# Kernel optimization log

Measured on AMD Instinct MI355X. Metric: run time of the kernel, lower is better.

Reference implementation:

```python
import jax, jax.numpy as jnp
import numpy as np

K = 3          # kernel size (hardcoded in module)
PAD = 1        # kernel_size // 2
K2 = K * K


def conv3x3(x, w, b):
    """Standard 3x3 stride-1 same-padding conv, NCHW / OIHW."""
    y = jax.lax.conv_general_dilated(
        x, w, window_strides=(1, 1), padding=[(PAD, PAD), (PAD, PAD)],
        dimension_numbers=('NCHW', 'OIHW', 'NCHW'))
    return y + b[None, :, None, None]


def setup_inputs() -> dict:
    key = jax.random.key(0)
    ks = jax.random.split(key, 8)
    B, C, O, H, W = 8, 64, 64, 128, 128
    x = jax.random.normal(ks[0], (B, C, H, W), dtype=jnp.float32)
    # offset conv: 2*K2 output channels; small init so offsets stay modest
    w_off = jax.random.normal(ks[1], (2 * K2, C, K, K), dtype=jnp.float32) * 0.05
    b_off = jnp.zeros((2 * K2,), dtype=jnp.float32)
    # modulator conv: K2 output channels
    w_mod = jax.random.normal(ks[2], (K2, C, K, K), dtype=jnp.float32) * 0.05
    b_mod = jnp.zeros((K2,), dtype=jnp.float32)
    # main deformable conv weight/bias
    w = jax.random.normal(ks[3], (O, C, K, K), dtype=jnp.float32) * (1.0 / np.sqrt(C * K2))
    b = jax.random.normal(ks[4], (O,), dtype=jnp.float32) * 0.01
    return {"x": x, "w_off": w_off, "b_off": b_off,
            "w_mod": w_mod, "b_mod": b_mod, "w": w, "b": b}


def reference(x, w_off, b_off, w_mod, b_mod, w, b):
    B, C, H, W = x.shape
    O = w.shape[0]

    # offset / modulator heads (torchvision layout: channel 2k = dy, 2k+1 = dx)
    offset = conv3x3(x, w_off, b_off)                       # [B, 2*K2, H, W]
    mask = 2.0 * jax.nn.sigmoid(conv3x3(x, w_mod, b_mod))   # [B, K2, H, W]
    off = offset.reshape(B, K2, 2, H, W)
    dy, dx = off[:, :, 0], off[:, :, 1]                     # [B, K2, H, W]

    # base sampling grid: p = (h - pad + ki, w - pad + kj) + learned offset
    ki = (jnp.arange(K2) // K).astype(x.dtype)
    kj = (jnp.arange(K2) % K).astype(x.dtype)
    hh = jnp.arange(H, dtype=x.dtype)
    ww = jnp.arange(W, dtype=x.dtype)
    py = dy + hh[None, None, :, None] - PAD + ki[None, :, None, None]
    px = dx + ww[None, None, None, :] - PAD + kj[None, :, None, None]

    def sample_one(x_b, py_b, px_b):
        # x_b: [C, H, W]; py_b, px_b: [K2, H, W]. Bilinear, zero outside.
        y0 = jnp.floor(py_b)
        x0 = jnp.floor(px_b)
        wy = py_b - y0                                      # [K2, H, W]
        wx = px_b - x0
        y0i = y0.astype(jnp.int32)
        x0i = x0.astype(jnp.int32)

        def gather(yi, xi):
            valid = (yi >= 0) & (yi < H) & (xi >= 0) & (xi < W)
            v = x_b[:, jnp.clip(yi, 0, H - 1), jnp.clip(xi, 0, W - 1)]  # [C,K2,H,W]
            return v * valid[None].astype(x_b.dtype)

        v00 = gather(y0i, x0i)
        v01 = gather(y0i, x0i + 1)
        v10 = gather(y0i + 1, x0i)
        v11 = gather(y0i + 1, x0i + 1)
        return (v00 * (1 - wy) * (1 - wx) + v01 * (1 - wy) * wx
                + v10 * wy * (1 - wx) + v11 * wy * wx)       # [C, K2, H, W]

    sampled = jax.vmap(sample_one)(x, py, px)               # [B, C, K2, H, W]

    # modulated contraction over (c, k): GEMM-like core
    wk = w.reshape(O, C, K2)
    out = jnp.einsum('bckhw,bkhw,ock->bohw', sampled, mask, wk)
    return out + b[None, :, None, None]
```

## Files before the change

### kernel.cpp

```cpp
#include <hip/hip_runtime.h>
#include <math.h>

#define H_ 128
#define W_ 128
#define C_ 64
#define O_ 64
#define B_ 8
#define K2_ 9
#define HWSZ (H_*W_)

typedef float f2u __attribute__((ext_vector_type(2), aligned(4)));

__global__ __launch_bounds__(256) void prep_weights_k(
    const float* __restrict__ w, const float* __restrict__ w_off,
    const float* __restrict__ w_mod, float* __restrict__ wt,
    float* __restrict__ wom) {
    int id = blockIdx.x * 256 + threadIdx.x;
    if (id < K2_ * C_ * O_) {
        int o = id & (O_ - 1);
        int c = (id >> 6) & (C_ - 1);
        int k = id / (C_ * O_);
        wt[id] = w[(o * C_ + c) * K2_ + k];
    }
    int id2 = id - K2_ * C_ * O_;
    if (id2 >= 0 && id2 < C_ * 243) {
        int k = id2 % 9;
        int tt = (id2 / 9) % 27;
        int c = id2 / 243;
        float v = (tt < 18) ? w_off[(tt * C_ + c) * K2_ + k]
                            : w_mod[((tt - 18) * C_ + c) * K2_ + k];
        wom[id2] = v;
    }
}

__global__ __launch_bounds__(512) void conv_offmask_k(
    const float* __restrict__ x,
    const float* __restrict__ wom, const float* __restrict__ b_off,
    const float* __restrict__ b_mod,
    float* __restrict__ pyA, float* __restrict__ pxA, float* __restrict__ mA) {
    __shared__ float red[27 * 128];

    int b     = blockIdx.x & 7;
    int strip = blockIdx.x >> 3;
    int tid   = threadIdx.x;
    int t     = tid & 127;
    int q     = tid >> 7;
    int c0    = __builtin_amdgcn_readfirstlane(q << 4);
    int p     = strip * 128 + t;
    int w     = p & (W_ - 1);
    int h     = p >> 7;

    int offs[9];
    float valid[9];
#pragma unroll
    for (int i = 0; i < 9; i++) {
        int dy = i / 3 - 1, dx = i % 3 - 1;
        int yy = h + dy, xx = w + dx;
        bool v = (yy >= 0 && yy < H_ && xx >= 0 && xx < W_);
        int yc = min(max(yy, 0), H_ - 1);
        int xc = min(max(xx, 0), W_ - 1);
        offs[i] = yc * W_ + xc;
        valid[i] = v ? 1.0f : 0.0f;
    }

    float acc[27];
#pragma unroll
    for (int o = 0; o < 27; o++) acc[o] = 0.0f;

    const float* xb = x + (b * C_ + c0) * HWSZ;

    float v[9];
#pragma unroll
    for (int i = 0; i < 9; i++) v[i] = xb[offs[i]] * valid[i];

    for (int c = 0; c < 16; c++) {
        const float* xn = xb + min(c + 1, 15) * HWSZ;
        float vn[9];
#pragma unroll
        for (int i = 0; i < 9; i++) vn[i] = xn[offs[i]] * valid[i];

        const float* wc = wom + (c0 + c) * 243;
#pragma unroll
        for (int o = 0; o < 27; o++) {
#pragma unroll
            for (int kk = 0; kk < 9; kk++) acc[o] += v[kk] * wc[o * 9 + kk];
        }
#pragma unroll
        for (int i = 0; i < 9; i++) v[i] = vn[i];
    }

    if (q == 3) {
#pragma unroll
        for (int o = 0; o < 27; o++) red[o * 128 + t] = acc[o];
    }
    __syncthreads();
    if (q == 2) {
#pragma unroll
        for (int o = 0; o < 27; o++) red[o * 128 + t] += acc[o];
    }
    __syncthreads();
    if (q == 1) {
#pragma unroll
        for (int o = 0; o < 27; o++) red[o * 128 + t] += acc[o];
    }
    __syncthreads();
    if (q == 0) {
#pragma unroll
        for (int k = 0; k < 9; k++) {
            float dy = acc[2 * k]     + red[(2 * k)     * 128 + t] + b_off[2 * k];
            float dx = acc[2 * k + 1] + red[(2 * k + 1) * 128 + t] + b_off[2 * k + 1];
            float mm = acc[18 + k]    + red[(18 + k)    * 128 + t] + b_mod[k];
            float mask = 2.0f / (1.0f + __expf(-mm));
            float py = dy + (float)h - 1.0f + (float)(k / 3);
            float px = dx + (float)w - 1.0f + (float)(k % 3);
            int idx = (b * 9 + k) * HWSZ + p;
            pyA[idx] = py;
            pxA[idx] = px;
            mA[idx] = mask;
        }
    }
}

__global__ __launch_bounds__(512) void sample_gemm_k(
    const float* __restrict__ x,
    const float* __restrict__ pyA, const float* __restrict__ pxA,
    const float* __restrict__ mA, const float* __restrict__ wt,
    const float* __restrict__ bias, float* __restrict__ out) {
    __shared__ float red[O_ * 256];

    int b     = blockIdx.x & 7;
    int strip = blockIdx.x >> 3;
    int tid   = threadIdx.x;
    int t     = tid & 255;
    int half  = tid >> 8;
    int c0    = __builtin_amdgcn_readfirstlane(half << 5);
    int p     = strip * 256 + t;

    float acc[O_];
#pragma unroll
    for (int o = 0; o < O_; o++) acc[o] = 0.0f;

    const float* xb = x + (b * C_ + c0) * HWSZ;

    for (int k = 0; k < 9; k++) {
        int idx = (b * 9 + k) * HWSZ + p;
        float py = pyA[idx];
        float px = pxA[idx];
        float m  = mA[idx];

        float y0f = floorf(py), x0f = floorf(px);
        float wy = py - y0f, wx = px - x0f;
        int y0 = (int)y0f, x0 = (int)x0f;
        int y1 = y0 + 1;
        float vy0 = (y0 >= 0 && y0 < H_) ? 1.0f : 0.0f;
        float vy1 = (y1 >= 0 && y1 < H_) ? 1.0f : 0.0f;
        float vx0 = (x0 >= 0 && x0 < W_) ? 1.0f : 0.0f;
        float vx1 = (x0 >= -1 && x0 < W_ - 1) ? 1.0f : 0.0f;
        int y0c = min(max(y0, 0), H_ - 1), y1c = min(max(y1, 0), H_ - 1);

        float w00 = (1.0f - wy) * (1.0f - wx) * vy0 * vx0 * m;
        float w01 = (1.0f - wy) * wx * vy0 * vx1 * m;
        float w10 = wy * (1.0f - wx) * vy1 * vx0 * m;
        float w11 = wy * wx * vy1 * vx1 * m;

        int lc   = min(max(x0, 0), W_ - 2);
        bool xlo = (x0 < 0);
        bool xhi = (x0 > W_ - 2);
        float a00 = xhi ? 0.0f : (xlo ? w01 : w00);
        float a01 = xlo ? 0.0f : (xhi ? w00 : w01);
        float a10 = xhi ? 0.0f : (xlo ? w11 : w10);
        float a11 = xlo ? 0.0f : (xhi ? w10 : w11);

        int r0 = y0c * W_ + lc;
        int r1 = y1c * W_ + lc;

        const float* wp = wt + k * (C_ * O_) + c0 * O_;
        for (int c = 0; c < 32; c++) {
            const float* xc = xb + c * HWSZ;
            f2u f0 = *(const f2u*)(xc + r0);
            f2u f1 = *(const f2u*)(xc + r1);
            float s = a00 * f0.x + a01 * f0.y + a10 * f1.x + a11 * f1.y;
            const float* wpc = wp + c * O_;
#pragma unroll
            for (int o = 0; o < O_; o++) acc[o] += s * wpc[o];
        }
    }

    if (half) {
#pragma unroll
        for (int o = 0; o < O_; o++) red[o * 256 + t] = acc[o];
    }
    __syncthreads();
    if (!half) {
        int obase = b * O_ * HWSZ + p;
#pragma unroll
        for (int o = 0; o < O_; o++)
            out[obase + o * HWSZ] = acc[o] + red[o * 256 + t] + bias[o];
    }
}

extern "C" void kernel_launch(void* const* d_in, const int* in_sizes, int n_in,
                              void* d_out, int out_size, void* d_ws, size_t ws_size,
                              hipStream_t stream) {
    const float* x     = (const float*)d_in[0];
    const float* w_off = (const float*)d_in[1];
    const float* b_off = (const float*)d_in[2];
    const float* w_mod = (const float*)d_in[3];
    const float* b_mod = (const float*)d_in[4];
    const float* w     = (const float*)d_in[5];
    const float* bias  = (const float*)d_in[6];
    float* out = (float*)d_out;

    const int nCoord = B_ * K2_ * HWSZ;
    float* pyA = (float*)d_ws;
    float* pxA = pyA + nCoord;
    float* mA  = pxA + nCoord;
    float* wt  = mA + nCoord;
    float* wom = wt + K2_ * C_ * O_;

    const int nPrep = K2_ * C_ * O_ + C_ * 243;
    hipLaunchKernelGGL(prep_weights_k, dim3((nPrep + 255) / 256), dim3(256),
                       0, stream, w, w_off, w_mod, wt, wom);
    hipLaunchKernelGGL(conv_offmask_k, dim3(1024), dim3(512), 0, stream,
                       x, wom, b_off, b_mod, pyA, pxA, mA);
    hipLaunchKernelGGL(sample_gemm_k, dim3(512), dim3(512), 0, stream,
                       x, pyA, pxA, mA, wt, bias, out);
}
```

Baseline: 321.6 us.

## Fuse offset/mask conv into deformable sampling GEMM kernel via shared memory

Merges the offset/modulator convolution kernel into the sampling+GEMM kernel. Each block first computes py/px/mask for its 256 pixels over two channel halves, reduces them in LDS, and keeps them there instead of writing them to global workspace. This removes a launch and the global round-trip of three B*9*H*W arrays. In exchange, the conv stage now runs on only 512 blocks with 32 channels per thread rather than 1024 blocks with 16, so it has less parallelism. The added launch-bounds occupancy hint may also pressure registers given the 64-wide accumulator.

```diff
diff --git a/kernel.cpp b/kernel.cpp
--- a/kernel.cpp
+++ b/kernel.cpp
@@ -33,98 +33,10 @@
     }
 }
 
-__global__ __launch_bounds__(512) void conv_offmask_k(
+__global__ __launch_bounds__(512, 4) void deform_fused_k(
     const float* __restrict__ x,
     const float* __restrict__ wom, const float* __restrict__ b_off,
-    const float* __restrict__ b_mod,
-    float* __restrict__ pyA, float* __restrict__ pxA, float* __restrict__ mA) {
-    __shared__ float red[27 * 128];
-
-    int b     = blockIdx.x & 7;
-    int strip = blockIdx.x >> 3;
-    int tid   = threadIdx.x;
-    int t     = tid & 127;
-    int q     = tid >> 7;
-    int c0    = __builtin_amdgcn_readfirstlane(q << 4);
-    int p     = strip * 128 + t;
-    int w     = p & (W_ - 1);
-    int h     = p >> 7;
-
-    int offs[9];
-    float valid[9];
-#pragma unroll
-    for (int i = 0; i < 9; i++) {
-        int dy = i / 3 - 1, dx = i % 3 - 1;
-        int yy = h + dy, xx = w + dx;
-        bool v = (yy >= 0 && yy < H_ && xx >= 0 && xx < W_);
-        int yc = min(max(yy, 0), H_ - 1);
-        int xc = min(max(xx, 0), W_ - 1);
-        offs[i] = yc * W_ + xc;
-        valid[i] = v ? 1.0f : 0.0f;
-    }
-
-    float acc[27];
-#pragma unroll
-    for (int o = 0; o < 27; o++) acc[o] = 0.0f;
-
-    const float* xb = x + (b * C_ + c0) * HWSZ;
-
-    float v[9];
-#pragma unroll
-    for (int i = 0; i < 9; i++) v[i] = xb[offs[i]] * valid[i];
-
-    for (int c = 0; c < 16; c++) {
-        const float* xn = xb + min(c + 1, 15) * HWSZ;
-        float vn[9];
-#pragma unroll
-        for (int i = 0; i < 9; i++) vn[i] = xn[offs[i]] * valid[i];
-
-        const float* wc = wom + (c0 + c) * 243;
-#pragma unroll
-        for (int o = 0; o < 27; o++) {
-#pragma unroll
-            for (int kk = 0; kk < 9; kk++) acc[o] += v[kk] * wc[o * 9 + kk];
-        }
-#pragma unroll
-        for (int i = 0; i < 9; i++) v[i] = vn[i];
-    }
-
-    if (q == 3) {
-#pragma unroll
-        for (int o = 0; o < 27; o++) red[o * 128 + t] = acc[o];
-    }
-    __syncthreads();
-    if (q == 2) {
-#pragma unroll
-        for (int o = 0; o < 27; o++) red[o * 128 + t] += acc[o];
-    }
-    __syncthreads();
-    if (q == 1) {
-#pragma unroll
-        for (int o = 0; o < 27; o++) red[o * 128 + t] += acc[o];
-    }
-    __syncthreads();
-    if (q == 0) {
-#pragma unroll
-        for (int k = 0; k < 9; k++) {
-            float dy = acc[2 * k]     + red[(2 * k)     * 128 + t] + b_off[2 * k];
-            float dx = acc[2 * k + 1] + red[(2 * k + 1) * 128 + t] + b_off[2 * k + 1];
-            float mm = acc[18 + k]    + red[(18 + k)    * 128 + t] + b_mod[k];
-            float mask = 2.0f / (1.0f + __expf(-mm));
-            float py = dy + (float)h - 1.0f + (float)(k / 3);
-            float px = dx + (float)w - 1.0f + (float)(k % 3);
-            int idx = (b * 9 + k) * HWSZ + p;
-            pyA[idx] = py;
-            pxA[idx] = px;
-            mA[idx] = mask;
-        }
-    }
-}
-
-__global__ __launch_bounds__(512) void sample_gemm_k(
-    const float* __restrict__ x,
-    const float* __restrict__ pyA, const float* __restrict__ pxA,
-    const float* __restrict__ mA, const float* __restrict__ wt,
+    const float* __restrict__ b_mod, const float* __restrict__ wt,
     const float* __restrict__ bias, float* __restrict__ out) {
     __shared__ float red[O_ * 256];
 
@@ -135,18 +47,79 @@
     int half  = tid >> 8;
     int c0    = __builtin_amdgcn_readfirstlane(half << 5);
     int p     = strip * 256 + t;
+    int w     = p & (W_ - 1);
+    int h     = p >> 7;
+
+    const float* xb = x + (b * C_ + c0) * HWSZ;
+
+    {
+        int offs[9];
+        float valid[9];
+#pragma unroll
+        for (int i = 0; i < 9; i++) {
+            int dy = i / 3 - 1, dx = i % 3 - 1;
+            int yy = h + dy, xx = w + dx;
+            bool v = (yy >= 0 && yy < H_ && xx >= 0 && xx < W_);
+            int yc = min(max(yy, 0), H_ - 1);
+            int xc = min(max(xx, 0), W_ - 1);
+            offs[i] = yc * W_ + xc;
+            valid[i] = v ? 1.0f : 0.0f;
+        }
+
+        float acc27[27];
+#pragma unroll
+        for (int o = 0; o < 27; o++) acc27[o] = 0.0f;
+
+        float v[9];
+#pragma unroll
+        for (int i = 0; i < 9; i++) v[i] = xb[offs[i]] * valid[i];
+
+        for (int c = 0; c < 32; c++) {
+            const float* xn = xb + min(c + 1, 31) * HWSZ;
+            float vn[9];
+#pragma unroll
+            for (int i = 0; i < 9; i++) vn[i] = xn[offs[i]] * valid[i];
+
+            const float* wc = wom + (c0 + c) * 243;
+#pragma unroll
+            for (int o = 0; o < 27; o++) {
+#pragma unroll
+                for (int kk = 0; kk < 9; kk++) acc27[o] += v[kk] * wc[o * 9 + kk];
+            }
+#pragma unroll
+            for (int i = 0; i < 9; i++) v[i] = vn[i];
+        }
+
+        if (half) {
+#pragma unroll
+            for (int o = 0; o < 27; o++) red[o * 256 + t] = acc27[o];
+        }
+        __syncthreads();
+        if (!half) {
+#pragma unroll
+            for (int k = 0; k < 9; k++) {
+                float dy = acc27[2 * k]     + red[(2 * k)     * 256 + t] + b_off[2 * k];
+                float dx = acc27[2 * k + 1] + red[(2 * k + 1) * 256 + t] + b_off[2 * k + 1];
+                float mm = acc27[18 + k]    + red[(18 + k)    * 256 + t] + b_mod[k];
+                float mask = 2.0f / (1.0f + __expf(-mm));
+                float py = dy + (float)h - 1.0f + (float)(k / 3);
+                float px = dx + (float)w - 1.0f + (float)(k % 3);
+                red[(27 + 3 * k + 0) * 256 + t] = py;
+                red[(27 + 3 * k + 1) * 256 + t] = px;
+                red[(27 + 3 * k + 2) * 256 + t] = mask;
+            }
+        }
+        __syncthreads();
+    }
 
     float acc[O_];
 #pragma unroll
     for (int o = 0; o < O_; o++) acc[o] = 0.0f;
 
-    const float* xb = x + (b * C_ + c0) * HWSZ;
-
     for (int k = 0; k < 9; k++) {
-        int idx = (b * 9 + k) * HWSZ + p;
-        float py = pyA[idx];
-        float px = pxA[idx];
-        float m  = mA[idx];
+        float py = red[(27 + 3 * k + 0) * 256 + t];
+        float px = red[(27 + 3 * k + 1) * 256 + t];
+        float m  = red[(27 + 3 * k + 2) * 256 + t];
 
         float y0f = floorf(py), x0f = floorf(px);
         float wy = py - y0f, wx = px - x0f;
@@ -186,6 +159,7 @@
         }
     }
 
+    __syncthreads();
     if (half) {
 #pragma unroll
         for (int o = 0; o < O_; o++) red[o * 256 + t] = acc[o];
@@ -211,18 +185,12 @@
     const float* bias  = (const float*)d_in[6];
     float* out = (float*)d_out;
 
-    const int nCoord = B_ * K2_ * HWSZ;
-    float* pyA = (float*)d_ws;
-    float* pxA = pyA + nCoord;
-    float* mA  = pxA + nCoord;
-    float* wt  = mA + nCoord;
+    float* wt  = (float*)d_ws;
     float* wom = wt + K2_ * C_ * O_;
 
     const int nPrep = K2_ * C_ * O_ + C_ * 243;
     hipLaunchKernelGGL(prep_weights_k, dim3((nPrep + 255) / 256), dim3(256),
                        0, stream, w, w_off, w_mod, wt, wom);
-    hipLaunchKernelGGL(conv_offmask_k, dim3(1024), dim3(512), 0, stream,
-                       x, wom, b_off, b_mod, pyA, pxA, mA);
-    hipLaunchKernelGGL(sample_gemm_k, dim3(512), dim3(512), 0, stream,
-                       x, pyA, pxA, mA, wt, bias, out);
+    hipLaunchKernelGGL(deform_fused_k, dim3(512), dim3(512), 0, stream,
+                       x, wom, b_off, b_mod, wt, bias, out);
 }
```

After: 350.7 us. 9.1% more time.

## Split offset conv by output channels and compute two rows per block

Applied to the files above, without the earlier changes.

The offset/mask conv kernel now divides work across the four thread groups by output channel (7 of 28 padded outputs each) rather than by input channel. Each thread computes two output rows, reusing a 4x3 input window across both. This removes the serial three-stage shared-memory reduction and halves the block count. The weight layout is padded to 28 outputs, and each thread now loops over all 64 input channels with fewer accumulators, so there are more loads per thread but better reuse of input rows.

```diff
diff --git a/kernel.cpp b/kernel.cpp
--- a/kernel.cpp
+++ b/kernel.cpp
@@ -23,99 +23,100 @@
         wt[id] = w[(o * C_ + c) * K2_ + k];
     }
     int id2 = id - K2_ * C_ * O_;
-    if (id2 >= 0 && id2 < C_ * 243) {
+    if (id2 >= 0 && id2 < C_ * 252) {
         int k = id2 % 9;
-        int tt = (id2 / 9) % 27;
-        int c = id2 / 243;
-        float v = (tt < 18) ? w_off[(tt * C_ + c) * K2_ + k]
-                            : w_mod[((tt - 18) * C_ + c) * K2_ + k];
+        int tt = (id2 / 9) % 28;
+        int c = id2 / 252;
+        float v = 0.0f;
+        if (tt < 18)      v = w_off[(tt * C_ + c) * K2_ + k];
+        else if (tt < 27) v = w_mod[((tt - 18) * C_ + c) * K2_ + k];
         wom[id2] = v;
     }
 }
 
-__global__ __launch_bounds__(512) void conv_offmask_k(
+__global__ __launch_bounds__(512, 4) void conv_offmask_k(
     const float* __restrict__ x,
     const float* __restrict__ wom, const float* __restrict__ b_off,
     const float* __restrict__ b_mod,
     float* __restrict__ pyA, float* __restrict__ pxA, float* __restrict__ mA) {
-    __shared__ float red[27 * 128];
+    __shared__ float AO[28 * 256];
 
     int b     = blockIdx.x & 7;
     int strip = blockIdx.x >> 3;
     int tid   = threadIdx.x;
     int t     = tid & 127;
     int q     = tid >> 7;
-    int c0    = __builtin_amdgcn_readfirstlane(q << 4);
-    int p     = strip * 128 + t;
-    int w     = p & (W_ - 1);
-    int h     = p >> 7;
-
-    int offs[9];
-    float valid[9];
-#pragma unroll
-    for (int i = 0; i < 9; i++) {
-        int dy = i / 3 - 1, dx = i % 3 - 1;
-        int yy = h + dy, xx = w + dx;
-        bool v = (yy >= 0 && yy < H_ && xx >= 0 && xx < W_);
-        int yc = min(max(yy, 0), H_ - 1);
-        int xc = min(max(xx, 0), W_ - 1);
-        offs[i] = yc * W_ + xc;
-        valid[i] = v ? 1.0f : 0.0f;
-    }
-
-    float acc[27];
-#pragma unroll
-    for (int o = 0; o < 27; o++) acc[o] = 0.0f;
-
-    const float* xb = x + (b * C_ + c0) * HWSZ;
-
-    float v[9];
-#pragma unroll
-    for (int i = 0; i < 9; i++) v[i] = xb[offs[i]] * valid[i];
-
-    for (int c = 0; c < 16; c++) {
-        const float* xn = xb + min(c + 1, 15) * HWSZ;
-        float vn[9];
-#pragma unroll
-        for (int i = 0; i < 9; i++) vn[i] = xn[offs[i]] * valid[i];
-
-        const float* wc = wom + (c0 + c) * 243;
-#pragma unroll
-        for (int o = 0; o < 27; o++) {
-#pragma unroll
-            for (int kk = 0; kk < 9; kk++) acc[o] += v[kk] * wc[o * 9 + kk];
-        }
-#pragma unroll
-        for (int i = 0; i < 9; i++) v[i] = vn[i];
-    }
-
-    if (q == 3) {
-#pragma unroll
-        for (int o = 0; o < 27; o++) red[o * 128 + t] = acc[o];
+    int qu    = __builtin_amdgcn_readfirstlane(q);
+    int h0    = strip * 2;
+
+    int offs[12]; float valid[12];
+#pragma unroll
+    for (int r = 0; r < 4; r++) {
+#pragma unroll
+        for (int cx = 0; cx < 3; cx++) {
+            int yy = h0 - 1 + r, xx = t - 1 + cx;
+            bool vv = (yy >= 0 && yy < H_ && xx >= 0 && xx < W_);
+            int yc = min(max(yy, 0), H_ - 1);
+            int xc = min(max(xx, 0), W_ - 1);
+            offs[r * 3 + cx] = yc * W_ + xc;
+            valid[r * 3 + cx] = vv ? 1.0f : 0.0f;
+        }
+    }
+
+    float acc0[7], acc1[7];
+#pragma unroll
+    for (int o = 0; o < 7; o++) { acc0[o] = 0.0f; acc1[o] = 0.0f; }
+
+    const float* xb = x + b * C_ * HWSZ;
+
+    float v[12];
+#pragma unroll
+    for (int i = 0; i < 12; i++) v[i] = xb[offs[i]] * valid[i];
+
+    for (int c = 0; c < C_; c++) {
+        const float* xn = xb + min(c + 1, C_ - 1) * HWSZ;
+        float vn[12];
+#pragma unroll
+        for (int i = 0; i < 12; i++) vn[i] = xn[offs[i]] * valid[i];
+
+        const float* wq = wom + c * 252 + qu * 63;
+#pragma unroll
+        for (int o = 0; o < 7; o++) {
+#pragma unroll
+            for (int kk = 0; kk < 9; kk++) {
+                float wv = wq[o * 9 + kk];
+                int ki = kk / 3, kj = kk % 3;
+                acc0[o] += v[ki * 3 + kj] * wv;
+                acc1[o] += v[(ki + 1) * 3 + kj] * wv;
+            }
+        }
+#pragma unroll
+        for (int i = 0; i < 12; i++) v[i] = vn[i];
+    }
+
+#pragma unroll
+    for (int o = 0; o < 7; o++) {
+        AO[(qu * 7 + o) * 256 + t]       = acc0[o];
+        AO[(qu * 7 + o) * 256 + 128 + t] = acc1[o];
     }
     __syncthreads();
-    if (q == 2) {
-#pragma unroll
-        for (int o = 0; o < 27; o++) red[o * 128 + t] += acc[o];
-    }
-    __syncthreads();
-    if (q == 1) {
-#pragma unroll
-        for (int o = 0; o < 27; o++) red[o * 128 + t] += acc[o];
-    }
-    __syncthreads();
-    if (q == 0) {
+
+    if (tid < 256) {
+        int px = tid;
+        int hh = h0 + (px >> 7);
+        int ww = px & 127;
+        int p  = hh * W_ + ww;
 #pragma unroll
         for (int k = 0; k < 9; k++) {
-            float dy = acc[2 * k]     + red[(2 * k)     * 128 + t] + b_off[2 * k];
-            float dx = acc[2 * k + 1] + red[(2 * k + 1) * 128 + t] + b_off[2 * k + 1];
-            float mm = acc[18 + k]    + red[(18 + k)    * 128 + t] + b_mod[k];
+            float dy = AO[(2 * k) * 256 + px]     + b_off[2 * k];
+            float dx = AO[(2 * k + 1) * 256 + px] + b_off[2 * k + 1];
+            float mm = AO[(18 + k) * 256 + px]    + b_mod[k];
             float mask = 2.0f / (1.0f + __expf(-mm));
-            float py = dy + (float)h - 1.0f + (float)(k / 3);
-            float px = dx + (float)w - 1.0f + (float)(k % 3);
+            float py = dy + (float)hh - 1.0f + (float)(k / 3);
+            float px_ = dx + (float)ww - 1.0f + (float)(k % 3);
             int idx = (b * 9 + k) * HWSZ + p;
             pyA[idx] = py;
-            pxA[idx] = px;
+            pxA[idx] = px_;
             mA[idx] = mask;
         }
     }
@@ -218,10 +219,10 @@
     float* wt  = mA + nCoord;
     float* wom = wt + K2_ * C_ * O_;
 
-    const int nPrep = K2_ * C_ * O_ + C_ * 243;
+    const int nPrep = K2_ * C_ * O_ + C_ * 252;
     hipLaunchKernelGGL(prep_weights_k, dim3((nPrep + 255) / 256), dim3(256),
                        0, stream, w, w_off, w_mod, wt, wom);
-    hipLaunchKernelGGL(conv_offmask_k, dim3(1024), dim3(512), 0, stream,
+    hipLaunchKernelGGL(conv_offmask_k, dim3(512), dim3(512), 0, stream,
                        x, wom, b_off, b_mod, pyA, pxA, mA);
     hipLaunchKernelGGL(sample_gemm_k, dim3(512), dim3(512), 0, stream,
                        x, pyA, pxA, mA, wt, bias, out);
```

New measurement: 303.6 us. 5.6% less time.
